# Performance work log

Hardware: AMD Instinct MI355X
Metric: run time of the kernel (lower is better)

The kernel has to match this reference:

```python
import jax, jax.numpy as jnp
import numpy as np

BINS = 10
LOSS_WEIGHT = 1.0


def setup_inputs() -> dict:
    key = jax.random.key(0)
    k1, k2 = jax.random.split(key)
    B, C = 16384, 1000
    logits = jax.random.normal(k1, (B, C), dtype=jnp.float32)
    target_indices = jax.random.randint(k2, (B,), 0, C)
    return {"logits": logits, "target_indices": target_indices}


def reference(logits, target_indices):
    B, C = logits.shape
    bins = BINS
    target = jax.nn.one_hot(target_indices, C, dtype=logits.dtype)  # [B, C]
    # gradient-norm proxy (detached in the original)
    g = jnp.abs(jax.nn.sigmoid(jax.lax.stop_gradient(logits)) - target)  # [B, C], in [0, 1]
    tot = jnp.asarray(B * C, logits.dtype)  # all label_weights are 1 -> tot = B*C
    # edges are i/bins with last edge bumped by 1e-6, so bin = clip(floor(g*bins), 0, bins-1)
    bin_idx = jnp.clip((g * bins).astype(jnp.int32), 0, bins - 1)  # [B, C]
    counts = jax.ops.segment_sum(
        jnp.ones((B * C,), logits.dtype), bin_idx.reshape(-1), num_segments=bins
    )  # [bins]
    nonempty = counts > 0
    n = jnp.sum(nonempty).astype(logits.dtype)  # number of non-empty bins
    per_bin_w = jnp.where(nonempty, tot / jnp.maximum(counts, 1.0), 0.0)  # [bins]
    weights = per_bin_w[bin_idx] / jnp.maximum(n, 1.0)  # [B, C]
    weights = jax.lax.stop_gradient(weights)
    # binary_cross_entropy_with_logits, elementwise, stable form
    bce = jnp.maximum(logits, 0.0) - logits * target + jnp.log1p(jnp.exp(-jnp.abs(logits)))
    loss = jnp.sum(weights * bce) / tot
    return loss * LOSS_WEIGHT
```

## Files before the change

### kernel.cpp

```cpp
#include <hip/hip_runtime.h>

typedef float v2f __attribute__((ext_vector_type(2)));

namespace {
constexpr int kB = 16384;
constexpr int kC = 1000;
constexpr int kNElem = kB * kC;
constexpr int kNV4 = kNElem / 4;
constexpr int kV4PerRow = kC / 4;
constexpr int kBlocks = 1280;
constexpr int kThreads = 256;
constexpr int kS = kBlocks * kThreads;
}


__device__ __forceinline__ void ghmc_elem(float L, float& bce, unsigned& bin)
{
    const float kLn2   = 0.6931471805599453f;
    const float kNRLn2 = -1.4426950408889634f;
    const float en  = __builtin_amdgcn_exp2f(kNRLn2 * fabsf(L));
    const float den = 1.f + en;
    const float lg  = __builtin_amdgcn_logf(den);
    const float r   = __builtin_amdgcn_rcpf(den);
    bce = fmaf(lg, kLn2, fmaxf(L, 0.f));
    unsigned babs = (unsigned)(10.f * r);
    babs = babs > 9u ? 9u : babs;
    bin = (L >= 0.f) ? babs : 9u - babs;
}

__device__ __forceinline__ void proc4(const float4 v, int dt,
    v2f& a01, v2f& a23, v2f& a45, v2f& a67, v2f& a89,
    unsigned long long& hcnt,
    const v2f C01, const v2f C23, const v2f C45, const v2f C67, const v2f C89)
{
    const float lv[4] = {v.x, v.y, v.z, v.w};
    #pragma unroll
    for (int e = 0; e < 4; ++e) {
        float bce; unsigned bin;
        ghmc_elem(lv[e], bce, bin);
        hcnt += 1ull << (6u * bin);
        const v2f b2 = {bce, bce};
        a01 += __builtin_elementwise_max(b2, C01);
        a23 += __builtin_elementwise_max(b2, C23);
        a45 += __builtin_elementwise_max(b2, C45);
        a67 += __builtin_elementwise_max(b2, C67);
        a89 += __builtin_elementwise_max(b2, C89);
    }
    if (__builtin_expect((unsigned)dt < 4u, 0)) {
        float L = v.x;
        L = (dt == 1) ? v.y : L;
        L = (dt == 2) ? v.z : L;
        L = (dt == 3) ? v.w : L;
        float bn_; unsigned bnb;
        ghmc_elem(L, bn_, bnb);
        const float bt_ = bn_ - L;
        const unsigned babs = (bnb >= 5u) ? bnb : 9u - bnb;
        const unsigned btb  = (L <= 0.f) ? babs : 9u - babs;
        hcnt += (1ull << (6u * btb)) - (1ull << (6u * bnb));
        const v2f bn2 = {bn_, bn_}, bt2 = {bt_, bt_};
        a01 += __builtin_elementwise_max(bt2, C01) - __builtin_elementwise_max(bn2, C01);
        a23 += __builtin_elementwise_max(bt2, C23) - __builtin_elementwise_max(bn2, C23);
        a45 += __builtin_elementwise_max(bt2, C45) - __builtin_elementwise_max(bn2, C45);
        a67 += __builtin_elementwise_max(bt2, C67) - __builtin_elementwise_max(bn2, C67);
        a89 += __builtin_elementwise_max(bt2, C89) - __builtin_elementwise_max(bn2, C89);
    }
}

__global__ __launch_bounds__(kThreads) void ghmc_main(
    const float* __restrict__ logits,
    const int* __restrict__ tgt,
    float* __restrict__ pf,
    unsigned* __restrict__ pu)
{
    const v2f C01 = {0.0f,        0.10536052f};
    const v2f C23 = {0.22314355f, 0.35667494f};
    const v2f C45 = {0.51082562f, 0.69314718f};
    const v2f C67 = {0.91629073f, 1.20397280f};
    const v2f C89 = {1.60943791f, 2.30258509f};

    v2f a01 = {0.f,0.f}, a23 = {0.f,0.f}, a45 = {0.f,0.f},
        a67 = {0.f,0.f}, a89 = {0.f,0.f};
    unsigned long long hcnt = 0ull;

    const int gid = blockIdx.x * blockDim.x + threadIdx.x;
    const int n = (kNV4 - 1 - gid) / kS + 1;
    const float4* __restrict__ Lp = reinterpret_cast<const float4*>(logits);

    auto ld = [&](int idx) {
        idx = idx < kNV4 ? idx : kNV4 - 1;
        return Lp[idx];
    };
    auto dtf = [&](int idx) {
        idx = idx < kNV4 ? idx : kNV4 - 1;
        const int row = idx / kV4PerRow;
        return tgt[row] - (idx - row * kV4PerRow) * 4;
    };

    int i = gid;
    float4 q0 = ld(i), q1 = ld(i + kS), q2 = ld(i + 2 * kS);
    int    d0 = dtf(i), d1 = dtf(i + kS), d2 = dtf(i + 2 * kS);

    int k = 0;
    for (; k + 4 <= n; k += 4) {
        float4 q3 = ld(i + 3 * kS);
        int    d3 = dtf(i + 3 * kS);
        proc4(q0, d0, a01, a23, a45, a67, a89, hcnt, C01, C23, C45, C67, C89);
        q0 = ld(i + 4 * kS);
        d0 = dtf(i + 4 * kS);
        proc4(q1, d1, a01, a23, a45, a67, a89, hcnt, C01, C23, C45, C67, C89);
        q1 = ld(i + 5 * kS);
        d1 = dtf(i + 5 * kS);
        proc4(q2, d2, a01, a23, a45, a67, a89, hcnt, C01, C23, C45, C67, C89);
        q2 = ld(i + 6 * kS);
        d2 = dtf(i + 6 * kS);
        proc4(q3, d3, a01, a23, a45, a67, a89, hcnt, C01, C23, C45, C67, C89);
        i += 4 * kS;
    }
    if (k < n) {
        proc4(q0, d0, a01, a23, a45, a67, a89, hcnt, C01, C23, C45, C67, C89);
    }

    unsigned long long lo = 0ull, hi = 0ull;
    #pragma unroll
    for (int j = 0; j < 5; ++j) {
        lo += ((hcnt >> (6 * j))       & 63ull) << (12 * j);
        hi += ((hcnt >> (6 * (j + 5))) & 63ull) << (12 * j);
    }
    float r10[10] = {a01.x, a01.y, a23.x, a23.y, a45.x, a45.y, a67.x, a67.y, a89.x, a89.y};
    #pragma unroll
    for (int off = 32; off > 0; off >>= 1) {
        #pragma unroll
        for (int j = 0; j < 10; ++j) r10[j] += __shfl_down(r10[j], off);
        lo += __shfl_down(lo, off);
        hi += __shfl_down(hi, off);
    }

    __shared__ float              sf[4][10];
    __shared__ unsigned long long sc[4][2];
    const int wave = threadIdx.x >> 6;
    const int lane = threadIdx.x & 63;
    if (lane == 0) {
        #pragma unroll
        for (int j = 0; j < 10; ++j) sf[wave][j] = r10[j];
        sc[wave][0] = lo; sc[wave][1] = hi;
    }
    __syncthreads();
    const int t = threadIdx.x;
    if (t < 10) {
        pf[t * kBlocks + blockIdx.x] = sf[0][t] + sf[1][t] + sf[2][t] + sf[3][t];
    } else if (t < 20) {
        const int b = t - 10;
        const int half = (b < 5) ? 0 : 1;
        const int sh = 12 * (b < 5 ? b : b - 5);
        unsigned s = 0;
        #pragma unroll
        for (int w = 0; w < 4; ++w) s += (unsigned)((sc[w][half] >> sh) & 4095ull);
        pu[b * kBlocks + blockIdx.x] = s;
    }
}

__global__ __launch_bounds__(640) void ghmc_reduce(
    const float* __restrict__ pf,
    const unsigned* __restrict__ pu,
    float* __restrict__ out)
{
    const int wave = threadIdx.x >> 6;
    const int lane = threadIdx.x & 63;

    double   fs = 0.0;
    unsigned cs = 0u;
    #pragma unroll 8
    for (int b = lane; b < kBlocks; b += 64) {
        fs += (double)pf[wave * kBlocks + b];
        cs += pu[wave * kBlocks + b];
    }
    #pragma unroll
    for (int off = 32; off > 0; off >>= 1) {
        fs += __shfl_down(fs, off);
        cs += __shfl_down(cs, off);
    }

    __shared__ double   sF[10];
    __shared__ unsigned sC[10];
    if (lane == 0) { sF[wave] = fs; sC[wave] = cs; }
    __syncthreads();

    if (threadIdx.x == 0) {
        const double cj[10] = {0.0,
            0.10536051565782630, 0.22314355131420976, 0.35667494393873245,
            0.51082562376599072, 0.69314718055994531, 0.91629073187415511,
            1.20397280432593600, 1.60943791243410040, 2.30258509299404570};
        double N[10], cnt[11], cum[11];
        for (int j = 0; j < 10; ++j) N[j] = (double)sC[j];
        cnt[10] = 0.0;
        for (int j = 9; j >= 0; --j) cnt[j] = cnt[j + 1] + N[j];
        cum[10] = 0.0;
        cum[0] = sF[0];
        for (int j = 1; j <= 9; ++j)
            cum[j] = sF[j] - cj[j] * ((double)kNElem - cnt[j]);
        double loss = 0.0, n = 0.0;
        for (int j = 0; j < 10; ++j) {
            if (N[j] > 0.0) { n += 1.0; loss += (cum[j] - cum[j + 1]) / N[j]; }
        }
        out[0] = (float)(loss / (n > 1.0 ? n : 1.0));
    }
}

extern "C" void kernel_launch(void* const* d_in, const int* in_sizes, int n_in,
                              void* d_out, int out_size, void* d_ws, size_t ws_size,
                              hipStream_t stream)
{
    const float* logits = (const float*)d_in[0];
    const int*   tgt    = (const int*)d_in[1];
    float*    pf = (float*)d_ws;
    unsigned* pu = (unsigned*)((char*)d_ws + 10 * kBlocks * 4);
    ghmc_main<<<kBlocks, kThreads, 0, stream>>>(logits, tgt, pf, pu);
    ghmc_reduce<<<1, 640, 0, stream>>>(pf, pu, (float*)d_out);
}
```

Before: 33.38 us.

## Fuse final reduction into main kernel via last-block atomic counter

Removes the separate single-block reduce kernel. Each block publishes its partials with atomic stores and bumps a global counter, and the last block to arrive performs the final reduction and loss computation. The target-offset calculation is also moved inline next to each proc4 call instead of being software-pipelined alongside the loads. This trades a kernel launch for a hipMemsetAsync of the counter plus atomic overhead, and the tail block still does the serial reduction.

```diff
diff --git a/kernel.cpp b/kernel.cpp
--- a/kernel.cpp
+++ b/kernel.cpp
@@ -70,7 +70,9 @@
     const float* __restrict__ logits,
     const int* __restrict__ tgt,
     float* __restrict__ pf,
-    unsigned* __restrict__ pu)
+    unsigned* __restrict__ pu,
+    unsigned* __restrict__ ctr,
+    float* __restrict__ out)
 {
     const v2f C01 = {0.0f,        0.10536052f};
     const v2f C23 = {0.22314355f, 0.35667494f};
@@ -90,34 +92,28 @@
         idx = idx < kNV4 ? idx : kNV4 - 1;
         return Lp[idx];
     };
-    auto dtf = [&](int idx) {
-        idx = idx < kNV4 ? idx : kNV4 - 1;
+    auto dtf = [&](const float4*, int idx) {
         const int row = idx / kV4PerRow;
         return tgt[row] - (idx - row * kV4PerRow) * 4;
     };
 
     int i = gid;
     float4 q0 = ld(i), q1 = ld(i + kS), q2 = ld(i + 2 * kS);
-    int    d0 = dtf(i), d1 = dtf(i + kS), d2 = dtf(i + 2 * kS);
 
     int k = 0;
     for (; k + 4 <= n; k += 4) {
         float4 q3 = ld(i + 3 * kS);
-        int    d3 = dtf(i + 3 * kS);
-        proc4(q0, d0, a01, a23, a45, a67, a89, hcnt, C01, C23, C45, C67, C89);
+        proc4(q0, dtf(Lp, i),          a01, a23, a45, a67, a89, hcnt, C01, C23, C45, C67, C89);
         q0 = ld(i + 4 * kS);
-        d0 = dtf(i + 4 * kS);
-        proc4(q1, d1, a01, a23, a45, a67, a89, hcnt, C01, C23, C45, C67, C89);
+        proc4(q1, dtf(Lp, i + kS),     a01, a23, a45, a67, a89, hcnt, C01, C23, C45, C67, C89);
         q1 = ld(i + 5 * kS);
-        d1 = dtf(i + 5 * kS);
-        proc4(q2, d2, a01, a23, a45, a67, a89, hcnt, C01, C23, C45, C67, C89);
+        proc4(q2, dtf(Lp, i + 2 * kS), a01, a23, a45, a67, a89, hcnt, C01, C23, C45, C67, C89);
         q2 = ld(i + 6 * kS);
-        d2 = dtf(i + 6 * kS);
-        proc4(q3, d3, a01, a23, a45, a67, a89, hcnt, C01, C23, C45, C67, C89);
+        proc4(q3, dtf(Lp, i + 3 * kS), a01, a23, a45, a67, a89, hcnt, C01, C23, C45, C67, C89);
         i += 4 * kS;
     }
     if (k < n) {
-        proc4(q0, d0, a01, a23, a45, a67, a89, hcnt, C01, C23, C45, C67, C89);
+        proc4(q0, dtf(Lp, i), a01, a23, a45, a67, a89, hcnt, C01, C23, C45, C67, C89);
     }
 
     unsigned long long lo = 0ull, hi = 0ull;
@@ -145,9 +141,12 @@
         sc[wave][0] = lo; sc[wave][1] = hi;
     }
     __syncthreads();
+
     const int t = threadIdx.x;
     if (t < 10) {
-        pf[t * kBlocks + blockIdx.x] = sf[0][t] + sf[1][t] + sf[2][t] + sf[3][t];
+        const float v = sf[0][t] + sf[1][t] + sf[2][t] + sf[3][t];
+        __hip_atomic_store(&pf[t * kBlocks + blockIdx.x], v,
+                           __ATOMIC_RELAXED, __HIP_MEMORY_SCOPE_AGENT);
     } else if (t < 20) {
         const int b = t - 10;
         const int half = (b < 5) ? 0 : 1;
@@ -155,54 +154,59 @@
         unsigned s = 0;
         #pragma unroll
         for (int w = 0; w < 4; ++w) s += (unsigned)((sc[w][half] >> sh) & 4095ull);
-        pu[b * kBlocks + blockIdx.x] = s;
-    }
-}
-
-__global__ __launch_bounds__(640) void ghmc_reduce(
-    const float* __restrict__ pf,
-    const unsigned* __restrict__ pu,
-    float* __restrict__ out)
-{
-    const int wave = threadIdx.x >> 6;
-    const int lane = threadIdx.x & 63;
-
-    double   fs = 0.0;
-    unsigned cs = 0u;
-    #pragma unroll 8
-    for (int b = lane; b < kBlocks; b += 64) {
-        fs += (double)pf[wave * kBlocks + b];
-        cs += pu[wave * kBlocks + b];
-    }
-    #pragma unroll
-    for (int off = 32; off > 0; off >>= 1) {
-        fs += __shfl_down(fs, off);
-        cs += __shfl_down(cs, off);
-    }
-
-    __shared__ double   sF[10];
-    __shared__ unsigned sC[10];
-    if (lane == 0) { sF[wave] = fs; sC[wave] = cs; }
-    __syncthreads();
-
-    if (threadIdx.x == 0) {
+        __hip_atomic_store(&pu[b * kBlocks + blockIdx.x], s,
+                           __ATOMIC_RELAXED, __HIP_MEMORY_SCOPE_AGENT);
+    }
+    __syncthreads();
+
+    __shared__ int s_last;
+    if (t == 0) {
+        const unsigned prev = __hip_atomic_fetch_add(
+            ctr, 1u, __ATOMIC_ACQ_REL, __HIP_MEMORY_SCOPE_AGENT);
+        s_last = (prev == (unsigned)(kBlocks - 1));
+    }
+    __syncthreads();
+    if (!s_last) return;
+
+    __shared__ double             rF[10];
+    __shared__ unsigned long long rC[10];
+    #pragma unroll
+    for (int s = wave; s < 10; s += 4) {
+        double fs = 0.0;
+        unsigned long long cs = 0ull;
+        for (int b = lane; b < kBlocks; b += 64) {
+            fs += (double)__hip_atomic_load(&pf[s * kBlocks + b],
+                                            __ATOMIC_RELAXED, __HIP_MEMORY_SCOPE_AGENT);
+            cs += __hip_atomic_load(&pu[s * kBlocks + b],
+                                    __ATOMIC_RELAXED, __HIP_MEMORY_SCOPE_AGENT);
+        }
+        #pragma unroll
+        for (int off = 32; off > 0; off >>= 1) {
+            fs += __shfl_down(fs, off);
+            cs += __shfl_down(cs, off);
+        }
+        if (lane == 0) { rF[s] = fs; rC[s] = cs; }
+    }
+    __syncthreads();
+
+    if (t == 0) {
         const double cj[10] = {0.0,
             0.10536051565782630, 0.22314355131420976, 0.35667494393873245,
             0.51082562376599072, 0.69314718055994531, 0.91629073187415511,
             1.20397280432593600, 1.60943791243410040, 2.30258509299404570};
         double N[10], cnt[11], cum[11];
-        for (int j = 0; j < 10; ++j) N[j] = (double)sC[j];
+        for (int j = 0; j < 10; ++j) N[j] = (double)rC[j];
         cnt[10] = 0.0;
         for (int j = 9; j >= 0; --j) cnt[j] = cnt[j + 1] + N[j];
         cum[10] = 0.0;
-        cum[0] = sF[0];
+        cum[0] = rF[0];
         for (int j = 1; j <= 9; ++j)
-            cum[j] = sF[j] - cj[j] * ((double)kNElem - cnt[j]);
-        double loss = 0.0, n = 0.0;
+            cum[j] = rF[j] - cj[j] * ((double)kNElem - cnt[j]);
+        double loss = 0.0, nn = 0.0;
         for (int j = 0; j < 10; ++j) {
-            if (N[j] > 0.0) { n += 1.0; loss += (cum[j] - cum[j + 1]) / N[j]; }
+            if (N[j] > 0.0) { nn += 1.0; loss += (cum[j] - cum[j + 1]) / N[j]; }
         }
-        out[0] = (float)(loss / (n > 1.0 ? n : 1.0));
+        out[0] = (float)(loss / (nn > 1.0 ? nn : 1.0));
     }
 }
 
@@ -212,8 +216,10 @@
 {
     const float* logits = (const float*)d_in[0];
     const int*   tgt    = (const int*)d_in[1];
-    float*    pf = (float*)d_ws;
-    unsigned* pu = (unsigned*)((char*)d_ws + 10 * kBlocks * 4);
-    ghmc_main<<<kBlocks, kThreads, 0, stream>>>(logits, tgt, pf, pu);
-    ghmc_reduce<<<1, 640, 0, stream>>>(pf, pu, (float*)d_out);
-}
+    float*    pf  = (float*)d_ws;
+    unsigned* pu  = (unsigned*)((char*)d_ws + 10 * kBlocks * 4);
+    unsigned* ctr = (unsigned*)((char*)d_ws + 20 * kBlocks * 4);
+    hipMemsetAsync(ctr, 0, 4, stream);
+    ghmc_main<<<kBlocks, kThreads, 0, stream>>>(logits, tgt, pf, pu, ctr,
+                                                (float*)d_out);
+}
```

New measurement: 74.00 us. 2.22x slower.
